# Kernel tuning notes

Hardware: AMD Instinct MI355X
Metric: run time of the kernel (lower is better)

## Reference

```python
import jax, jax.numpy as jnp
import numpy as np

N_CODES = 1024
D = 128
BETA = 0.25


def setup_inputs() -> dict:
    key = jax.random.key(0)
    k1, k2 = jax.random.split(key)
    z = jax.random.normal(k1, (8, D, 4096), dtype=jnp.float32)  # (B, D, T)
    # nn.init.uniform_(codebook.weight, -1/n_codes, 1/n_codes)
    codebook = jax.random.uniform(
        k2, (N_CODES, D), dtype=jnp.float32,
        minval=-1.0 / N_CODES, maxval=1.0 / N_CODES)
    return {"z": z, "codebook": codebook}


def reference(z, codebook):
    B, D_, T = z.shape
    z_t = jnp.transpose(z, (0, 2, 1))           # (B, T, D)
    flat = z_t.reshape(B * T, D_)               # (BT, D)
    dist = (jnp.sum(flat * flat, axis=1, keepdims=True)
            - 2.0 * flat @ codebook.T
            + jnp.sum(codebook * codebook, axis=1)[None, :])
    codes = jnp.argmin(dist, axis=1)            # (BT,)
    z_q = codebook[codes].reshape(B, T, D_)     # (B, T, D)
    commit = jnp.mean((z_t - jax.lax.stop_gradient(z_q)) ** 2)
    codebk = jnp.mean((z_q - jax.lax.stop_gradient(z_t)) ** 2)
    loss = codebk + BETA * commit
    # straight-through estimator
    z_q_st = z_t + jax.lax.stop_gradient(z_q - z_t)
    z_q_out = jnp.transpose(z_q_st, (0, 2, 1))  # (B, D, T)
    return (z_q_out, codes.reshape(B, T), loss,
            dist.reshape(B, T, codebook.shape[0]))
```

## Files before the change

kernel.cpp:

```cpp
#include <hip/hip_runtime.h>

typedef __attribute__((ext_vector_type(8))) short short8;
typedef __attribute__((ext_vector_type(4))) float f32x4;

namespace {
constexpr long long OFF_CODES = 4194304;
constexpr long long OFF_LOSS  = 4227072;
constexpr long long OFF_DIST  = 4227073;
constexpr float EPS = 5e-4f;
constexpr size_t WS_LACC = 0;
constexpr size_t WS_WCNT = 8;
constexpr size_t WS_SCF  = 1024;
constexpr size_t WS_SZF  = 8192;
constexpr size_t WS_WLST = 139264;
constexpr size_t WS_CBF  = 270336;
}

__device__ __forceinline__ unsigned short bf_rne(float v) {
  unsigned int u = __float_as_uint(v);
  unsigned int r = u + 0x7FFFu + ((u >> 16) & 1u);
  return (unsigned short)(r >> 16);
}

__global__ __launch_bounds__(256) void vq_cbfrag(
    const float* __restrict__ cb, unsigned short* __restrict__ cbf,
    float* __restrict__ scf, double* lacc, unsigned int* wcnt)
{
  __shared__ double pn[4][16];
  const int g = blockIdx.x;
  const int tid = threadIdx.x;
  const int ks = tid >> 6, l = tid & 63, lg = l >> 4, lj = l & 15;
  const float* src = cb + (size_t)(g * 16 + lj) * 128 + ks * 32 + lg * 8;
  double s = 0.0;
  short8 h;
#pragma unroll
  for (int e = 0; e < 8; ++e) {
    float v = src[e];
    float q = v * v;
    s += (double)q;
    h[e] = (short)bf_rne(v);
  }
  *reinterpret_cast<short8*>(cbf + (size_t)g * 2048 + (size_t)tid * 8) = h;
  s += __shfl_xor(s, 16);
  s += __shfl_xor(s, 32);
  if (lg == 0) pn[ks][lj] = s;
  __syncthreads();
  if (tid < 16)
    scf[g * 16 + tid] = (float)(pn[0][tid] + pn[1][tid] + pn[2][tid] + pn[3][tid]);
  if (blockIdx.x == 0 && tid == 0) { *lacc = 0.0; *wcnt = 0u; }
}

__global__ __launch_bounds__(256, 4) void vq_main(
    const float* __restrict__ z, const unsigned short* __restrict__ cbf,
    const float* __restrict__ cb, const float* __restrict__ scf,
    float* __restrict__ szf, unsigned int* __restrict__ wcnt,
    unsigned int* __restrict__ wlist, float* __restrict__ out,
    double* __restrict__ lacc)
{
  __shared__ __align__(16) unsigned short zh[32 * 136];
  __shared__ float cq[32 * 132];
  __shared__ double part[32][8];
  __shared__ float szl[32];
  __shared__ float scfl[1024];
  __shared__ float rm1[4][32], rm2[4][32];
  __shared__ int   ri1[4][32];
  __shared__ int   ci[32];
  __shared__ double lw[4];

  const int tid = threadIdx.x;
  const int R0 = blockIdx.x * 32;
  const int b = R0 >> 12, t0 = R0 & 4095;
  const float* zb = z + (size_t)b * 524288;

#pragma unroll
  for (int k = 0; k < 4; ++k) scfl[k * 256 + tid] = scf[k * 256 + tid];

  float zreg[16];
  {
    double ps = 0.0;
    const int t = tid & 31;
#pragma unroll
    for (int k = 0; k < 16; ++k) {
      int d = k * 8 + (tid >> 5);
      float v = zb[(size_t)d * 4096 + t0 + t];
      zreg[k] = v;
      float q = v * v;
      ps += (double)q;
      zh[t * 136 + d] = bf_rne(v);
    }
    part[t][tid >> 5] = ps;
  }
  __syncthreads();
  if (tid < 32) {
    double s = 0.0;
#pragma unroll
    for (int g = 0; g < 8; ++g) s += part[tid][g];
    float sz = (float)s;
    szl[tid] = sz;
    szf[R0 + tid] = sz;
  }
  __syncthreads();

  const int w = tid >> 6, l = tid & 63, lj = l & 15, lg = l >> 4;

  short8 Ah[2][4];
#pragma unroll
  for (int tt = 0; tt < 2; ++tt)
#pragma unroll
    for (int ks = 0; ks < 4; ++ks)
      Ah[tt][ks] = *reinterpret_cast<const short8*>(
          &zh[(tt * 16 + lj) * 136 + ks * 32 + lg * 8]);
  float szr[2][4];
#pragma unroll
  for (int tt = 0; tt < 2; ++tt)
#pragma unroll
    for (int r = 0; r < 4; ++r) szr[tt][r] = szl[tt * 16 + lg * 4 + r];

  float m1[8], m2[8]; int i1[8];
#pragma unroll
  for (int s = 0; s < 8; ++s) { m1[s] = 3.4e38f; m2[s] = 3.4e38f; i1[s] = 0; }

  const unsigned short* pwave = cbf + (size_t)w * 16 * 2048 + (size_t)l * 8;

#pragma unroll 1
  for (int q = 0; q < 4; ++q) {
    f32x4 acc[2][4];
#pragma unroll
    for (int u = 0; u < 4; ++u) {
      acc[0][u] = (f32x4){0.f, 0.f, 0.f, 0.f};
      acc[1][u] = (f32x4){0.f, 0.f, 0.f, 0.f};
      const unsigned short* pg = pwave + (size_t)(q * 4 + u) * 2048;
#pragma unroll
      for (int ks = 0; ks < 4; ++ks) {
        short8 bh = *reinterpret_cast<const short8*>(pg + ks * 512);
        acc[0][u] = __builtin_amdgcn_mfma_f32_16x16x32_bf16(Ah[0][ks], bh, acc[0][u], 0, 0, 0);
        acc[1][u] = __builtin_amdgcn_mfma_f32_16x16x32_bf16(Ah[1][ks], bh, acc[1][u], 0, 0, 0);
      }
    }
#pragma unroll
    for (int u = 0; u < 4; ++u) {
      const int jj = w * 256 + (q * 4 + u) * 16 + lj;
      const float sc = scfl[jj];
#pragma unroll
      for (int tt = 0; tt < 2; ++tt)
#pragma unroll
        for (int r = 0; r < 4; ++r) {
          float dv = (szr[tt][r] - 2.0f * acc[tt][u][r]) + sc;
          const int s = tt * 4 + r;
          bool lt1 = dv < m1[s];
          float o1 = m1[s];
          m2[s] = lt1 ? o1 : fminf(m2[s], dv);
          m1[s] = lt1 ? dv : o1;
          i1[s] = lt1 ? jj : i1[s];
          out[OFF_DIST + (size_t)(R0 + tt * 16 + lg * 4 + r) * 1024 + jj] = dv;
        }
    }
  }

#pragma unroll
  for (int s = 0; s < 8; ++s) {
    float a1 = m1[s]; int ai = i1[s]; float a2 = m2[s];
#pragma unroll
    for (int msk = 1; msk <= 8; msk <<= 1) {
      float b1 = __shfl_xor(a1, msk);
      int   bi = __shfl_xor(ai, msk);
      float b2 = __shfl_xor(a2, msk);
      bool keep = (a1 < b1) || (a1 == b1 && ai < bi);
      float lose = keep ? b1 : a1;
      a2 = fminf(fminf(a2, b2), lose);
      ai = keep ? ai : bi;
      a1 = keep ? a1 : b1;
    }
    if (lj == 0) {
      int t = (s >> 2) * 16 + lg * 4 + (s & 3);
      rm1[w][t] = a1; ri1[w][t] = ai; rm2[w][t] = a2;
    }
  }
  __syncthreads();
  if (tid < 32) {
    float f1 = rm1[0][tid]; int fi = ri1[0][tid]; float f2 = rm2[0][tid];
#pragma unroll
    for (int ww = 1; ww < 4; ++ww) {
      float b1 = rm1[ww][tid]; int bi = ri1[ww][tid]; float b2 = rm2[ww][tid];
      bool keep = (f1 < b1) || (f1 == b1 && fi < bi);
      float lose = keep ? b1 : f1;
      f2 = fminf(fminf(f2, b2), lose);
      fi = keep ? fi : bi;
      f1 = keep ? f1 : b1;
    }
    int R = R0 + tid;
    out[OFF_CODES + R] = (float)fi;
    ci[tid] = fi;
    if (f2 - f1 <= EPS) {
      unsigned int pos = atomicAdd(wcnt, 1u);
      wlist[pos] = (unsigned int)R;
    }
  }
  __syncthreads();

  {
    const int row = tid >> 3, p = tid & 7;
    const float* csrc = cb + (size_t)ci[row] * 128 + p * 16;
#pragma unroll
    for (int e = 0; e < 16; ++e) cq[row * 132 + p * 16 + e] = csrc[e];
  }
  __syncthreads();

  double ls = 0.0;
  {
    const int t = tid & 31, dg = tid >> 5;
    float* zq = out + (size_t)b * 524288 + t0 + t;
#pragma unroll
    for (int k = 0; k < 16; ++k) {
      int d = k * 8 + dg;
      float zv = zreg[k];
      float qv = cq[t * 132 + d];
      zq[(size_t)d * 4096] = zv + (qv - zv);
      double dd = (double)qv - (double)zv;
      ls += dd * dd;
    }
  }
#pragma unroll
  for (int msk = 1; msk <= 32; msk <<= 1) ls += __shfl_xor(ls, msk);
  if ((tid & 63) == 0) lw[tid >> 6] = ls;
  __syncthreads();
  if (tid == 0) atomicAdd(lacc, lw[0] + lw[1] + lw[2] + lw[3]);
}

__global__ __launch_bounds__(256) void vq_refine(
    const float* __restrict__ z, const float* __restrict__ cb,
    const float* __restrict__ scf, const float* __restrict__ szf,
    const unsigned int* __restrict__ wcnt, const unsigned int* __restrict__ wlist,
    float* __restrict__ out, double* __restrict__ lacc)
{
  const int w = threadIdx.x >> 6, l = threadIdx.x & 63;
  const unsigned int cnt = *wcnt;
  for (unsigned int i = blockIdx.x * 4 + w; i < cnt; i += 1024) {
    const int R = (int)wlist[i];
    const int b = R >> 12, t = R & 4095;

    const float* drow = out + OFF_DIST + (size_t)R * 1024;
    float v[16];
#pragma unroll
    for (int k = 0; k < 16; ++k) v[k] = drow[k * 64 + l];
    float mn = 3.4e38f;
#pragma unroll
    for (int k = 0; k < 16; ++k) mn = fminf(mn, v[k]);
#pragma unroll
    for (int msk = 1; msk <= 32; msk <<= 1) mn = fminf(mn, __shfl_xor(mn, msk));
    const float thresh = mn + EPS;

    const float zv0f = z[(size_t)b * 524288 + (size_t)l * 4096 + t];
    const float zv1f = z[(size_t)b * 524288 + (size_t)(l + 64) * 4096 + t];
    const double zd0 = (double)zv0f, zd1 = (double)zv1f;
    const float szv = szf[R];

    float bestv = 3.4e38f; int bestj = 1 << 30;
#pragma unroll
    for (int k = 0; k < 16; ++k) {
      unsigned long long msk = __ballot(v[k] <= thresh);
      while (msk) {
        int s = __ffsll((unsigned long long)msk) - 1;
        msk &= msk - 1;
        int jc = k * 64 + s;
        float c0 = cb[(size_t)jc * 128 + l];
        float c1 = cb[(size_t)jc * 128 + 64 + l];
        double m = zd0 * (double)c0 + zd1 * (double)c1;
#pragma unroll
        for (int mm = 1; mm <= 32; mm <<= 1) m += __shfl_xor(m, mm);
        float m32 = (float)m;
        float dvex = (szv - 2.0f * m32) + scf[jc];
        if (dvex < bestv || (dvex == bestv && jc < bestj)) { bestv = dvex; bestj = jc; }
      }
    }

    const int fiOld = (int)out[OFF_CODES + R];
    if (bestj != fiOld) {
      if (l == 0) out[OFF_CODES + R] = (float)bestj;
      float cn0 = cb[(size_t)bestj * 128 + l];
      float cn1 = cb[(size_t)bestj * 128 + 64 + l];
      float co0 = cb[(size_t)fiOld * 128 + l];
      float co1 = cb[(size_t)fiOld * 128 + 64 + l];
      float* zq = out + (size_t)b * 524288 + t;
      zq[(size_t)l * 4096]        = zv0f + (cn0 - zv0f);
      zq[(size_t)(l + 64) * 4096] = zv1f + (cn1 - zv1f);
      double dn0 = (double)cn0 - zd0, dn1 = (double)cn1 - zd1;
      double do0 = (double)co0 - zd0, do1 = (double)co1 - zd1;
      double dl = dn0 * dn0 + dn1 * dn1 - do0 * do0 - do1 * do1;
#pragma unroll
      for (int mm = 1; mm <= 32; mm <<= 1) dl += __shfl_xor(dl, mm);
      if (l == 0) atomicAdd(lacc, dl);
    }
  }
}

__global__ void vq_fin(const double* lacc, float* out) {
  if (threadIdx.x == 0 && blockIdx.x == 0)
    out[OFF_LOSS] = (float)(*lacc * (1.25 / 4194304.0));
}

extern "C" void kernel_launch(void* const* d_in, const int* in_sizes, int n_in,
                              void* d_out, int out_size, void* d_ws, size_t ws_size,
                              hipStream_t stream) {
  const float* z  = (const float*)d_in[0];
  const float* cb = (const float*)d_in[1];
  float* out = (float*)d_out;
  char* ws = (char*)d_ws;
  double* lacc = (double*)(ws + WS_LACC);
  unsigned int* wcnt = (unsigned int*)(ws + WS_WCNT);
  float* scf = (float*)(ws + WS_SCF);
  float* szf = (float*)(ws + WS_SZF);
  unsigned int* wlist = (unsigned int*)(ws + WS_WLST);
  unsigned short* cbf = (unsigned short*)(ws + WS_CBF);

  vq_cbfrag<<<64, 256, 0, stream>>>(cb, cbf, scf, lacc, wcnt);
  vq_main<<<1024, 256, 0, stream>>>(z, cbf, cb, scf, szf, wcnt, wlist, out, lacc);
  vq_refine<<<256, 256, 0, stream>>>(z, cb, scf, szf, wcnt, wlist, out, lacc);
  vq_fin<<<1, 64, 0, stream>>>(lacc, out);
}
```

Measured before the change: 88.34 us.

## Split VQ main kernel into distance/argmin and output kernels with transposed MFMA

Splits the fused kernel into a distance/argmin kernel over 16-row tiles and a separate kernel that gathers codebook rows and writes z_q and the loss. The MFMA operands are swapped so the codebook becomes the A operand. Each lane then holds four consecutive codes for one row, which allows 16-byte vectorised stores of the large distance matrix instead of scattered scalar stores. The cost is an extra launch, a re-read of z and of the codes from global memory, and lower MFMA reuse per codebook fragment since each block now covers 16 rows instead of 32.

```diff
diff --git a/kernel.cpp b/kernel.cpp
--- a/kernel.cpp
+++ b/kernel.cpp
@@ -50,118 +50,91 @@
   if (blockIdx.x == 0 && tid == 0) { *lacc = 0.0; *wcnt = 0u; }
 }
 
-__global__ __launch_bounds__(256, 4) void vq_main(
+__global__ __launch_bounds__(256, 4) void vq_dist(
     const float* __restrict__ z, const unsigned short* __restrict__ cbf,
-    const float* __restrict__ cb, const float* __restrict__ scf,
-    float* __restrict__ szf, unsigned int* __restrict__ wcnt,
-    unsigned int* __restrict__ wlist, float* __restrict__ out,
-    double* __restrict__ lacc)
-{
-  __shared__ __align__(16) unsigned short zh[32 * 136];
-  __shared__ float cq[32 * 132];
-  __shared__ double part[32][8];
-  __shared__ float szl[32];
+    const float* __restrict__ scf, float* __restrict__ szf,
+    unsigned int* __restrict__ wcnt, unsigned int* __restrict__ wlist,
+    float* __restrict__ out)
+{
+  __shared__ __align__(16) unsigned short zh[16 * 136];
+  __shared__ double part[16][16];
+  __shared__ float szl[16];
   __shared__ float scfl[1024];
-  __shared__ float rm1[4][32], rm2[4][32];
-  __shared__ int   ri1[4][32];
-  __shared__ int   ci[32];
-  __shared__ double lw[4];
+  __shared__ float rm1[4][16], rm2[4][16];
+  __shared__ int   ri1[4][16];
 
   const int tid = threadIdx.x;
-  const int R0 = blockIdx.x * 32;
-  const int b = R0 >> 12, t0 = R0 & 4095;
+  const int T0 = blockIdx.x * 16;
+  const int b = T0 >> 12, t0 = T0 & 4095;
   const float* zb = z + (size_t)b * 524288;
 
 #pragma unroll
   for (int k = 0; k < 4; ++k) scfl[k * 256 + tid] = scf[k * 256 + tid];
 
-  float zreg[16];
   {
+    const int t = tid & 15, dg = tid >> 4;
     double ps = 0.0;
-    const int t = tid & 31;
-#pragma unroll
-    for (int k = 0; k < 16; ++k) {
-      int d = k * 8 + (tid >> 5);
+#pragma unroll
+    for (int e = 0; e < 8; ++e) {
+      int d = e * 16 + dg;
       float v = zb[(size_t)d * 4096 + t0 + t];
-      zreg[k] = v;
       float q = v * v;
       ps += (double)q;
       zh[t * 136 + d] = bf_rne(v);
     }
-    part[t][tid >> 5] = ps;
-  }
-  __syncthreads();
-  if (tid < 32) {
+    part[t][dg] = ps;
+  }
+  __syncthreads();
+  if (tid < 16) {
     double s = 0.0;
 #pragma unroll
-    for (int g = 0; g < 8; ++g) s += part[tid][g];
+    for (int g = 0; g < 16; ++g) s += part[tid][g];
     float sz = (float)s;
     szl[tid] = sz;
-    szf[R0 + tid] = sz;
+    szf[T0 + tid] = sz;
   }
   __syncthreads();
 
   const int w = tid >> 6, l = tid & 63, lj = l & 15, lg = l >> 4;
 
-  short8 Ah[2][4];
-#pragma unroll
-  for (int tt = 0; tt < 2; ++tt)
-#pragma unroll
-    for (int ks = 0; ks < 4; ++ks)
-      Ah[tt][ks] = *reinterpret_cast<const short8*>(
-          &zh[(tt * 16 + lj) * 136 + ks * 32 + lg * 8]);
-  float szr[2][4];
-#pragma unroll
-  for (int tt = 0; tt < 2; ++tt)
-#pragma unroll
-    for (int r = 0; r < 4; ++r) szr[tt][r] = szl[tt * 16 + lg * 4 + r];
-
-  float m1[8], m2[8]; int i1[8];
-#pragma unroll
-  for (int s = 0; s < 8; ++s) { m1[s] = 3.4e38f; m2[s] = 3.4e38f; i1[s] = 0; }
-
+  short8 Bz[4];
+#pragma unroll
+  for (int ks = 0; ks < 4; ++ks)
+    Bz[ks] = *reinterpret_cast<const short8*>(&zh[lj * 136 + ks * 32 + lg * 8]);
+  const float szv = szl[lj];
+
+  float m1 = 3.4e38f, m2 = 3.4e38f; int i1 = 0;
   const unsigned short* pwave = cbf + (size_t)w * 16 * 2048 + (size_t)l * 8;
-
-#pragma unroll 1
-  for (int q = 0; q < 4; ++q) {
-    f32x4 acc[2][4];
-#pragma unroll
-    for (int u = 0; u < 4; ++u) {
-      acc[0][u] = (f32x4){0.f, 0.f, 0.f, 0.f};
-      acc[1][u] = (f32x4){0.f, 0.f, 0.f, 0.f};
-      const unsigned short* pg = pwave + (size_t)(q * 4 + u) * 2048;
-#pragma unroll
-      for (int ks = 0; ks < 4; ++ks) {
-        short8 bh = *reinterpret_cast<const short8*>(pg + ks * 512);
-        acc[0][u] = __builtin_amdgcn_mfma_f32_16x16x32_bf16(Ah[0][ks], bh, acc[0][u], 0, 0, 0);
-        acc[1][u] = __builtin_amdgcn_mfma_f32_16x16x32_bf16(Ah[1][ks], bh, acc[1][u], 0, 0, 0);
-      }
-    }
-#pragma unroll
-    for (int u = 0; u < 4; ++u) {
-      const int jj = w * 256 + (q * 4 + u) * 16 + lj;
-      const float sc = scfl[jj];
-#pragma unroll
-      for (int tt = 0; tt < 2; ++tt)
-#pragma unroll
-        for (int r = 0; r < 4; ++r) {
-          float dv = (szr[tt][r] - 2.0f * acc[tt][u][r]) + sc;
-          const int s = tt * 4 + r;
-          bool lt1 = dv < m1[s];
-          float o1 = m1[s];
-          m2[s] = lt1 ? o1 : fminf(m2[s], dv);
-          m1[s] = lt1 ? dv : o1;
-          i1[s] = lt1 ? jj : i1[s];
-          out[OFF_DIST + (size_t)(R0 + tt * 16 + lg * 4 + r) * 1024 + jj] = dv;
-        }
-    }
-  }
-
-#pragma unroll
-  for (int s = 0; s < 8; ++s) {
-    float a1 = m1[s]; int ai = i1[s]; float a2 = m2[s];
-#pragma unroll
-    for (int msk = 1; msk <= 8; msk <<= 1) {
+  float* orow = out + OFF_DIST + (size_t)(T0 + lj) * 1024 + w * 256 + lg * 4;
+
+#pragma unroll
+  for (int u = 0; u < 16; ++u) {
+    const unsigned short* pg = pwave + (size_t)u * 2048;
+    f32x4 a = (f32x4){0.f, 0.f, 0.f, 0.f};
+#pragma unroll
+    for (int ks = 0; ks < 4; ++ks) {
+      short8 af = *reinterpret_cast<const short8*>(pg + ks * 512);
+      a = __builtin_amdgcn_mfma_f32_16x16x32_bf16(af, Bz[ks], a, 0, 0, 0);
+    }
+    const int j0 = w * 256 + u * 16 + lg * 4;
+    f32x4 dvv;
+#pragma unroll
+    for (int r = 0; r < 4; ++r) {
+      float dv = (szv - 2.0f * a[r]) + scfl[j0 + r];
+      bool lt1 = dv < m1;
+      float o1 = m1;
+      m2 = lt1 ? o1 : fminf(m2, dv);
+      m1 = lt1 ? dv : o1;
+      i1 = lt1 ? (j0 + r) : i1;
+      dvv[r] = dv;
+    }
+    __builtin_memcpy(orow + u * 16, &dvv, 16);
+  }
+
+  {
+    float a1 = m1; int ai = i1; float a2 = m2;
+#pragma unroll
+    for (int msk = 16; msk <= 32; msk <<= 1) {
       float b1 = __shfl_xor(a1, msk);
       int   bi = __shfl_xor(ai, msk);
       float b2 = __shfl_xor(a2, msk);
@@ -171,13 +144,10 @@
       ai = keep ? ai : bi;
       a1 = keep ? a1 : b1;
     }
-    if (lj == 0) {
-      int t = (s >> 2) * 16 + lg * 4 + (s & 3);
-      rm1[w][t] = a1; ri1[w][t] = ai; rm2[w][t] = a2;
-    }
-  }
-  __syncthreads();
-  if (tid < 32) {
+    if (lg == 0) { rm1[w][lj] = a1; ri1[w][lj] = ai; rm2[w][lj] = a2; }
+  }
+  __syncthreads();
+  if (tid < 16) {
     float f1 = rm1[0][tid]; int fi = ri1[0][tid]; float f2 = rm2[0][tid];
 #pragma unroll
     for (int ww = 1; ww < 4; ++ww) {
@@ -188,37 +158,44 @@
       fi = keep ? fi : bi;
       f1 = keep ? f1 : b1;
     }
-    int R = R0 + tid;
+    int R = T0 + tid;
     out[OFF_CODES + R] = (float)fi;
-    ci[tid] = fi;
     if (f2 - f1 <= EPS) {
       unsigned int pos = atomicAdd(wcnt, 1u);
       wlist[pos] = (unsigned int)R;
     }
   }
-  __syncthreads();
-
-  {
-    const int row = tid >> 3, p = tid & 7;
-    const float* csrc = cb + (size_t)ci[row] * 128 + p * 16;
-#pragma unroll
-    for (int e = 0; e < 16; ++e) cq[row * 132 + p * 16 + e] = csrc[e];
-  }
-  __syncthreads();
-
+}
+
+__global__ __launch_bounds__(256) void vq_out_kernel(
+    const float* __restrict__ z, const float* __restrict__ cb,
+    float* __restrict__ out, double* __restrict__ lacc)
+{
+  __shared__ int ci[128];
+  __shared__ float cq[128][129];
+  __shared__ double lw[4];
+  const int tid = threadIdx.x;
+  const int b  = blockIdx.x >> 5;
+  const int t0 = (blockIdx.x & 31) * 128;
+  const int R0 = b * 4096 + t0;
+  if (tid < 128) ci[tid] = (int)out[OFF_CODES + R0 + tid];
+  __syncthreads();
+  for (int r = 0; r < 128; r += 2) {
+    int row = r + (tid >> 7);
+    int d = tid & 127;
+    cq[row][d] = cb[(size_t)ci[row] * 128 + d];
+  }
+  __syncthreads();
   double ls = 0.0;
-  {
-    const int t = tid & 31, dg = tid >> 5;
-    float* zq = out + (size_t)b * 524288 + t0 + t;
-#pragma unroll
-    for (int k = 0; k < 16; ++k) {
-      int d = k * 8 + dg;
-      float zv = zreg[k];
-      float qv = cq[t * 132 + d];
-      zq[(size_t)d * 4096] = zv + (qv - zv);
-      double dd = (double)qv - (double)zv;
-      ls += dd * dd;
-    }
+  for (int dp = 0; dp < 128; dp += 2) {
+    int d = dp + (tid >> 7);
+    int t = tid & 127;
+    size_t o = (size_t)b * 524288 + (size_t)d * 4096 + t0 + t;
+    float zv = z[o];
+    float q = cq[t][d];
+    out[o] = zv + (q - zv);
+    double dd = (double)q - (double)zv;
+    ls += dd * dd;
   }
 #pragma unroll
   for (int msk = 1; msk <= 32; msk <<= 1) ls += __shfl_xor(ls, msk);
@@ -314,7 +291,8 @@
   unsigned short* cbf = (unsigned short*)(ws + WS_CBF);
 
   vq_cbfrag<<<64, 256, 0, stream>>>(cb, cbf, scf, lacc, wcnt);
-  vq_main<<<1024, 256, 0, stream>>>(z, cbf, cb, scf, szf, wcnt, wlist, out, lacc);
+  vq_dist<<<2048, 256, 0, stream>>>(z, cbf, scf, szf, wcnt, wlist, out);
+  vq_out_kernel<<<256, 256, 0, stream>>>(z, cb, out, lacc);
   vq_refine<<<256, 256, 0, stream>>>(z, cb, scf, szf, wcnt, wlist, out, lacc);
   vq_fin<<<1, 64, 0, stream>>>(lacc, out);
 }
```

New measurement: 87.98 us. No clear change (-0.4%).

## Split quantized output write and loss into a separate kernel

Applied to the files above, without the earlier changes.

Moves the codebook gather, straight-through output write and loss accumulation out of vq_main into a new vq_out_kernel working on 128-row tiles. This removes the zreg registers, the cq shared array and two barriers from vq_main, which can raise its occupancy. The cost is an extra launch, a second read of z from global memory and a read-back of the codes. vq_refine runs after the new kernel, so refined rows are still overwritten correctly.

```diff
diff --git a/kernel.cpp b/kernel.cpp
--- a/kernel.cpp
+++ b/kernel.cpp
@@ -52,20 +52,16 @@
 
 __global__ __launch_bounds__(256, 4) void vq_main(
     const float* __restrict__ z, const unsigned short* __restrict__ cbf,
-    const float* __restrict__ cb, const float* __restrict__ scf,
-    float* __restrict__ szf, unsigned int* __restrict__ wcnt,
-    unsigned int* __restrict__ wlist, float* __restrict__ out,
-    double* __restrict__ lacc)
+    const float* __restrict__ scf, float* __restrict__ szf,
+    unsigned int* __restrict__ wcnt, unsigned int* __restrict__ wlist,
+    float* __restrict__ out)
 {
   __shared__ __align__(16) unsigned short zh[32 * 136];
-  __shared__ float cq[32 * 132];
   __shared__ double part[32][8];
   __shared__ float szl[32];
   __shared__ float scfl[1024];
   __shared__ float rm1[4][32], rm2[4][32];
   __shared__ int   ri1[4][32];
-  __shared__ int   ci[32];
-  __shared__ double lw[4];
 
   const int tid = threadIdx.x;
   const int R0 = blockIdx.x * 32;
@@ -75,7 +71,6 @@
 #pragma unroll
   for (int k = 0; k < 4; ++k) scfl[k * 256 + tid] = scf[k * 256 + tid];
 
-  float zreg[16];
   {
     double ps = 0.0;
     const int t = tid & 31;
@@ -83,7 +78,6 @@
     for (int k = 0; k < 16; ++k) {
       int d = k * 8 + (tid >> 5);
       float v = zb[(size_t)d * 4096 + t0 + t];
-      zreg[k] = v;
       float q = v * v;
       ps += (double)q;
       zh[t * 136 + d] = bf_rne(v);
@@ -190,35 +184,42 @@
     }
     int R = R0 + tid;
     out[OFF_CODES + R] = (float)fi;
-    ci[tid] = fi;
     if (f2 - f1 <= EPS) {
       unsigned int pos = atomicAdd(wcnt, 1u);
       wlist[pos] = (unsigned int)R;
     }
   }
-  __syncthreads();
-
-  {
-    const int row = tid >> 3, p = tid & 7;
-    const float* csrc = cb + (size_t)ci[row] * 128 + p * 16;
-#pragma unroll
-    for (int e = 0; e < 16; ++e) cq[row * 132 + p * 16 + e] = csrc[e];
-  }
-  __syncthreads();
-
+}
+
+__global__ __launch_bounds__(256) void vq_out_kernel(
+    const float* __restrict__ z, const float* __restrict__ cb,
+    float* __restrict__ out, double* __restrict__ lacc)
+{
+  __shared__ int ci[128];
+  __shared__ float cq[128][129];
+  __shared__ double lw[4];
+  const int tid = threadIdx.x;
+  const int b  = blockIdx.x >> 5;
+  const int t0 = (blockIdx.x & 31) * 128;
+  const int R0 = b * 4096 + t0;
+  if (tid < 128) ci[tid] = (int)out[OFF_CODES + R0 + tid];
+  __syncthreads();
+  for (int r = 0; r < 128; r += 2) {
+    int row = r + (tid >> 7);
+    int d = tid & 127;
+    cq[row][d] = cb[(size_t)ci[row] * 128 + d];
+  }
+  __syncthreads();
   double ls = 0.0;
-  {
-    const int t = tid & 31, dg = tid >> 5;
-    float* zq = out + (size_t)b * 524288 + t0 + t;
-#pragma unroll
-    for (int k = 0; k < 16; ++k) {
-      int d = k * 8 + dg;
-      float zv = zreg[k];
-      float qv = cq[t * 132 + d];
-      zq[(size_t)d * 4096] = zv + (qv - zv);
-      double dd = (double)qv - (double)zv;
-      ls += dd * dd;
-    }
+  for (int dp = 0; dp < 128; dp += 2) {
+    int d = dp + (tid >> 7);
+    int t = tid & 127;
+    size_t o = (size_t)b * 524288 + (size_t)d * 4096 + t0 + t;
+    float zv = z[o];
+    float q = cq[t][d];
+    out[o] = zv + (q - zv);
+    double dd = (double)q - (double)zv;
+    ls += dd * dd;
   }
 #pragma unroll
   for (int msk = 1; msk <= 32; msk <<= 1) ls += __shfl_xor(ls, msk);
@@ -314,7 +315,8 @@
   unsigned short* cbf = (unsigned short*)(ws + WS_CBF);
 
   vq_cbfrag<<<64, 256, 0, stream>>>(cb, cbf, scf, lacc, wcnt);
-  vq_main<<<1024, 256, 0, stream>>>(z, cbf, cb, scf, szf, wcnt, wlist, out, lacc);
+  vq_main<<<1024, 256, 0, stream>>>(z, cbf, scf, szf, wcnt, wlist, out);
+  vq_out_kernel<<<256, 256, 0, stream>>>(z, cb, out, lacc);
   vq_refine<<<256, 256, 0, stream>>>(z, cb, scf, szf, wcnt, wlist, out, lacc);
   vq_fin<<<1, 64, 0, stream>>>(lacc, out);
 }
```

Result: faster. 83.32 us (-5.7%).
